# Performance work log

Measured on AMD Instinct MI355X. Metric: run time of the kernel, lower is better.

Reference implementation:

```python
import jax, jax.numpy as jnp
import numpy as np

BINS = 10          # config.bins
SCOPE = 2          # config.dropout_scope_lowest (continue_train=True)
BASE_RATE = 0.0    # self.dropout_rate = zeros(1) when continue_train
THRESH = (BINS - SCOPE) / BINS   # edges[bins - dropout_scope]
UPPER = 1.0 + 1e-6               # edges[bins] (last edge += 1e-6)


def _forward(pred, target, rand_mat, hard_rand, pos_prop):
    B, C = pred.shape
    Bf = jnp.asarray(B, pred.dtype)
    # BCEWithLogits, reduction='none': logaddexp(0,x) - x*t
    bce = jnp.logaddexp(0.0, pred) - pred * target                     # [B,C]
    # g is detached in the torch code
    g = jax.lax.stop_gradient(jnp.abs(jax.nn.sigmoid(pred) - target))  # [B,C]
    # per-class loss -> normalized -> per-class dropout rate
    loss_c = bce.sum(0)                                                # [C]
    ln = jnp.log10(1.0 + loss_c)
    norm = 5.0 - 10.0 * (ln - ln.min()) / (ln.max() - ln.min())
    drate = jnp.maximum(jax.nn.sigmoid(norm), BASE_RATE)               # [C]
    # pos/neg balance bookkeeping (all per-class)
    pos_sum = target.sum(0)                                            # [C]
    neg_sum = Bf - pos_sum
    bal_pos = pos_prop * Bf
    bal_neg = Bf - bal_pos
    pos_gt = pos_sum > bal_pos                                         # majority is positives
    neg_gt = neg_sum > bal_neg                                         # majority is negatives
    balance_num = jnp.where(pos_gt, bal_pos, jnp.where(neg_gt, bal_neg, 0.0))
    dropout_num = jnp.floor(
        jnp.where(pos_gt, pos_sum - bal_pos,
                  jnp.where(neg_gt, neg_sum - bal_neg, 0.0))).astype(jnp.int32)
    # hard/easy class split: uniform(1,C) > dropout_rate
    hard = hard_rand[0] > drate                                        # [C] bool
    maj_lab = pos_gt.astype(pred.dtype)
    min_lab = neg_gt.astype(pred.dtype)
    is_maj = target == maj_lab[None, :]                                # [B,C]
    is_min = target == min_lab[None, :]
    maj_cnt = is_maj.sum(0).astype(pred.dtype)                         # [C]
    min_cnt = is_min.sum(0).astype(pred.dtype)
    # hard branch: reweight majority samples to balance_num/|majority|
    w_hard = jnp.where(is_maj, (balance_num / jnp.maximum(maj_cnt, 1.0))[None, :], 1.0)
    # easy branch: zero the dropout_num easiest (smallest g) majority samples,
    # rescale minority by (B - balance_num)/|minority|
    g_m = jnp.where(is_maj, g, jnp.inf)
    ranks = jnp.argsort(jnp.argsort(g_m, axis=0), axis=0)              # rank among majority by g asc
    drop_easy = is_maj & (ranks < dropout_num[None, :])
    w_easy = jnp.where(is_min & (min_cnt > 0)[None, :],
                       ((Bf - balance_num) / jnp.maximum(min_cnt, 1.0))[None, :], 1.0)
    w_easy = jnp.where(drop_easy, 0.0, w_easy)
    weights = jnp.where(hard[None, :], w_hard, w_easy)                 # [B,C]
    # random dropping of high-|g| (hard-gradient band) samples
    idxs = ((g >= THRESH) & (g < UPPER)).astype(pred.dtype)
    drop_idxs = (rand_mat > drate[None, :]).astype(pred.dtype)
    weights = weights * (1.0 - drop_idxs * idxs)
    return (bce * weights).mean()


def setup_inputs() -> dict:
    key = jax.random.key(0)
    k1, k2, k3, k4, k5 = jax.random.split(key, 5)
    B, C = 131072, 40
    pred = jax.random.normal(k1, (B, C), jnp.float32) * 2.0
    target = jax.random.bernoulli(k2, 0.5, (B, C)).astype(jnp.float32)
    rand_mat = jax.random.uniform(k3, (B, C), jnp.float32)
    hard_rand = jax.random.uniform(k4, (1, C), jnp.float32)
    pos_prop = jax.random.uniform(k5, (C,), jnp.float32, minval=0.3, maxval=0.7)
    return {"pred": pred, "target": target, "rand_mat": rand_mat,
            "hard_rand": hard_rand, "pos_prop": pos_prop}


def reference(pred, target, rand_mat, hard_rand, pos_prop):
    return _forward(pred, target, rand_mat, hard_rand, pos_prop)
```

## Files before the change

### kernel.cpp

```cpp
#include <hip/hip_runtime.h>
#include <hip/hip_bf16.h>
#include <math.h>
#include <stddef.h>

#define BN 131072
#define CN 40
#define NTOT (BN * CN)
#define MASKW (BN / 64)
#define NBLK 1024
#define NCHUNK 8
#define CROWS (BN / NCHUNK)

struct Ws {
    double acc;
    unsigned done;
    unsigned pad0;
    unsigned ghist0[CN][4096];
    unsigned ghist1[CN][1024];
    unsigned ghist2[CN][256];
    double lossc[CN];
    int    posc[CN];
    float drate[CN];
    float majl[CN];
    float minl[CN];
    float w_hard[CN];
    float w_easy[CN];
    int   hardf[CN];
    int   kdrop[CN];
    int   minpos[CN];
    union {
        unsigned long long mask[CN][MASKW];
        struct { float lpart[CN][NBLK]; int ppart[CN][NBLK]; } parts;
    } u;
    unsigned long long eqmask[CN][MASKW];
    unsigned keys[CN][BN];
};

__device__ __forceinline__ float bce_f(float x, float t) {
    float e = __expf(-fabsf(x));
    return fmaxf(x, 0.0f) + __logf(1.0f + e) - x * t;
}
__device__ __forceinline__ float g_f(float x, float t) {
    float e   = __expf(-fabsf(x));
    float inv = __builtin_amdgcn_rcpf(1.0f + e);
    float s   = (x >= 0.0f) ? inv : e * inv;
    return fabsf(s - t);
}
__device__ __forceinline__ void bce_g(float x, float t, float& bce, float& g) {
    float e   = __expf(-fabsf(x));
    bce       = fmaxf(x, 0.0f) + __logf(1.0f + e) - x * t;
    float inv = __builtin_amdgcn_rcpf(1.0f + e);
    float s   = (x >= 0.0f) ? inv : e * inv;
    g         = fabsf(s - t);
}
__device__ __forceinline__ unsigned masked_key(unsigned key, unsigned majb) {
    return ((key & 1u) == majb) ? (key >> 1) : 0xFFFFFFFFu;
}
__device__ __forceinline__ bool col_active(const Ws* ws, int c) {
    return (ws->kdrop[c] > 0) && (ws->hardf[c] == 0);
}

template<int PER, int NBINS>
__device__ __forceinline__ void scan_pick(const unsigned* __restrict__ gh,
                                          unsigned krem,
                                          unsigned* wsum ,
                                          unsigned* out2 ) {
    int tid = threadIdx.x, lane = tid & 63, w = tid >> 6;
    unsigned v[PER];
    unsigned s = 0;
    #pragma unroll
    for (int i = 0; i < PER; ++i) {
        int idx = tid * PER + i;
        v[i] = (idx < NBINS) ? gh[idx] : 0u;
        s += v[i];
    }
    unsigned isc = s;
    #pragma unroll
    for (int d = 1; d < 64; d <<= 1) {
        unsigned o = __shfl_up(isc, (unsigned)d, 64);
        if (lane >= d) isc += o;
    }
    if (lane == 63) wsum[w] = isc;
    __syncthreads();
    unsigned wpre = 0;
    #pragma unroll
    for (int j = 0; j < 16; ++j) wpre += (j < w) ? wsum[j] : 0u;
    unsigned inc = wpre + isc, prev = inc - s;
    if (prev < krem && inc >= krem) {
        unsigned cum = prev;
        #pragma unroll
        for (int i = 0; i < PER; ++i) {
            if (cum < krem && cum + v[i] >= krem) {
                out2[0] = (unsigned)(tid * PER + i);
                out2[1] = krem - cum;
            }
            cum += v[i];
        }
    }
    __syncthreads();
}

__global__ __launch_bounds__(640) void k_fuse(const float* __restrict__ pred,
                                              const float* __restrict__ tgt,
                                              Ws* __restrict__ ws) {
    __shared__ unsigned shk[128 * 41];
    __shared__ float sl[CN];
    __shared__ int   sp[CN];
    int tid = threadIdx.x;
    if (tid < CN) { sl[tid] = 0.0f; sp[tid] = 0; }
    __syncthreads();

    int  tile  = (blockIdx.x & 7) * 128 + (blockIdx.x >> 3);
    long tile0 = (long)tile * 5120;
    int  c0    = (tid * 4) % 40;
    float accl[4] = {0, 0, 0, 0};
    int   cntp[4] = {0, 0, 0, 0};

    #pragma unroll
    for (int j = 0; j < 2; ++j) {
        int e = j * 2560 + tid * 4;
        const float4 p = *(const float4*)(pred + tile0 + e);
        const float4 t = *(const float4*)(tgt + tile0 + e);
        int r = e / 40;
        #pragma unroll
        for (int u = 0; u < 4; ++u) {
            float pu = (&p.x)[u], tu = (&t.x)[u];
            float bce, g;
            bce_g(pu, tu, bce, g);
            accl[u] += bce;
            int tb = (tu != 0.0f) ? 1 : 0;
            cntp[u] += tb;
            shk[r * 41 + c0 + u] = (__float_as_uint(g) << 1) | (unsigned)tb;
        }
    }
    #pragma unroll
    for (int u = 0; u < 4; ++u) {
        atomicAdd(&sl[c0 + u], accl[u]);
        atomicAdd(&sp[c0 + u], cntp[u]);
    }
    __syncthreads();

    int w = tid / 128, r = tid % 128;
    int row0 = tile * 128;
    #pragma unroll
    for (int cc = 0; cc < 8; ++cc) {
        int c = w * 8 + cc;
        ws->keys[c][row0 + r] = shk[r * 41 + c];
    }
    if (tid < CN) {
        ws->u.parts.lpart[tid][blockIdx.x] = sl[tid];
        ws->u.parts.ppart[tid][blockIdx.x] = sp[tid];
    }
}

__global__ __launch_bounds__(1024) void k_sel0(const float* __restrict__ hard_rand,
                                               const float* __restrict__ pos_prop,
                                               Ws* __restrict__ ws) {
    const int bid = blockIdx.x;
    const int c = bid >> 3, chunk = bid & 7;
    const int tid = threadIdx.x, lane = tid & 63, wv = tid >> 6;

    __shared__ unsigned h[4096];
    __shared__ double s_lns[CN];
    __shared__ int s_pos;
    __shared__ int s_active, s_kdrop;
    __shared__ unsigned s_majb;

    for (int j = wv; j < CN; j += 16) {
        double s = 0.0;
        for (int q = lane; q < NBLK; q += 64)
            s += (double)ws->u.parts.lpart[j][q];
        #pragma unroll
        for (int d = 32; d >= 1; d >>= 1) s += __shfl_down(s, d, 64);
        if (lane == 0) s_lns[j] = log10(1.0 + s);
    }
    if (wv == 15) {
        int p = 0;
        for (int q = lane; q < NBLK; q += 64) p += ws->u.parts.ppart[c][q];
        #pragma unroll
        for (int d = 32; d >= 1; d >>= 1) p += __shfl_down(p, d, 64);
        if (lane == 0) s_pos = p;
    }
    __syncthreads();
    if (tid == 0) {
        double mn = s_lns[0], mx = s_lns[0];
        for (int i = 1; i < CN; ++i) { mn = fmin(mn, s_lns[i]); mx = fmax(mx, s_lns[i]); }
        double norm = 5.0 - 10.0 * (s_lns[c] - mn) / (mx - mn);
        float drate = (float)(1.0 / (1.0 + exp(-norm)));
        float Bf = (float)BN;
        float pos_sum = (float)s_pos;
        float neg_sum = Bf - pos_sum;
        float bal_pos = pos_prop[c] * Bf;
        float bal_neg = Bf - bal_pos;
        bool pos_gt = pos_sum > bal_pos;
        bool neg_gt = neg_sum > bal_neg;
        float balance = pos_gt ? bal_pos : (neg_gt ? bal_neg : 0.0f);
        float dnum_f  = pos_gt ? (pos_sum - bal_pos)
                               : (neg_gt ? (neg_sum - bal_neg) : 0.0f);
        int   kdrop   = (int)floorf(dnum_f);
        float majl = pos_gt ? 1.0f : 0.0f;
        float minl = neg_gt ? 1.0f : 0.0f;
        float maj_cnt = (majl == 1.0f) ? pos_sum : neg_sum;
        float min_cnt = (minl == 1.0f) ? pos_sum : neg_sum;
        int hardf = (hard_rand[c] > drate) ? 1 : 0;
        if (chunk == 0) {
            ws->drate[c]  = drate;
            ws->majl[c]   = majl;
            ws->minl[c]   = minl;
            ws->w_hard[c] = balance / fmaxf(maj_cnt, 1.0f);
            ws->w_easy[c] = (Bf - balance) / fmaxf(min_cnt, 1.0f);
            ws->hardf[c]  = hardf;
            ws->kdrop[c]  = kdrop;
            ws->minpos[c] = (min_cnt > 0.0f) ? 1 : 0;
        }
        s_active = (kdrop > 0 && hardf == 0) ? 1 : 0;
        s_kdrop  = kdrop;
        s_majb   = (majl != 0.0f) ? 1u : 0u;
    }
    __syncthreads();
    if (!s_active) return;
    const unsigned majb = s_majb;
    const uint4* kc4 = (const uint4*)(ws->keys[c] + chunk * CROWS);

    for (int i = tid; i < 4096; i += 1024) h[i] = 0;
    __syncthreads();
    for (int b4 = tid; b4 < CROWS / 4; b4 += 1024) {
        uint4 kk = kc4[b4];
        unsigned ks[4] = {kk.x, kk.y, kk.z, kk.w};
        #pragma unroll
        for (int q = 0; q < 4; ++q)
            if ((ks[q] & 1u) == majb) atomicAdd(&h[(ks[q] >> 1) >> 18], 1u);
    }
    __syncthreads();
    for (int i = tid; i < 4096; i += 1024)
        if (h[i]) atomicAdd(&ws->ghist0[c][i], h[i]);
}

__global__ __launch_bounds__(1024) void k_hist1(Ws* __restrict__ ws) {
    int c = blockIdx.x >> 3, chunk = blockIdx.x & 7;
    if (!col_active(ws, c)) return;
    __shared__ unsigned wsum[16];
    __shared__ unsigned out2[2];
    scan_pick<4, 4096>(ws->ghist0[c], (unsigned)ws->kdrop[c], wsum, out2);
    unsigned p0 = out2[0];
    unsigned majb = (ws->majl[c] != 0.0f) ? 1u : 0u;
    const uint4* __restrict__ kc4 = (const uint4*)(ws->keys[c] + chunk * CROWS);
    __shared__ unsigned h[1024];
    int tid = threadIdx.x;
    h[tid] = 0;
    __syncthreads();
    for (int b4 = tid; b4 < CROWS / 4; b4 += 1024) {
        uint4 kk = kc4[b4];
        unsigned ks[4] = {kk.x, kk.y, kk.z, kk.w};
        #pragma unroll
        for (int q = 0; q < 4; ++q)
            if ((ks[q] & 1u) == majb) {
                unsigned mk = ks[q] >> 1;
                if ((mk >> 18) == p0) atomicAdd(&h[(mk >> 8) & 0x3FFu], 1u);
            }
    }
    __syncthreads();
    if (h[tid]) atomicAdd(&ws->ghist1[c][tid], h[tid]);
}

__global__ __launch_bounds__(1024) void k_hist2(Ws* __restrict__ ws) {
    int c = blockIdx.x >> 3, chunk = blockIdx.x & 7;
    if (!col_active(ws, c)) return;
    __shared__ unsigned wsum[16];
    __shared__ unsigned out2[2];
    scan_pick<4, 4096>(ws->ghist0[c], (unsigned)ws->kdrop[c], wsum, out2);
    unsigned p0 = out2[0], krem1 = out2[1];
    scan_pick<1, 1024>(ws->ghist1[c], krem1, wsum, out2);
    unsigned pp = (p0 << 10) | out2[0];
    unsigned majb = (ws->majl[c] != 0.0f) ? 1u : 0u;
    const uint4* __restrict__ kc4 = (const uint4*)(ws->keys[c] + chunk * CROWS);
    __shared__ unsigned h[256];
    int tid = threadIdx.x;
    if (tid < 256) h[tid] = 0;
    __syncthreads();
    for (int b4 = tid; b4 < CROWS / 4; b4 += 1024) {
        uint4 kk = kc4[b4];
        unsigned ks[4] = {kk.x, kk.y, kk.z, kk.w};
        #pragma unroll
        for (int q = 0; q < 4; ++q)
            if ((ks[q] & 1u) == majb) {
                unsigned mk = ks[q] >> 1;
                if ((mk >> 8) == pp) atomicAdd(&h[mk & 0xFFu], 1u);
            }
    }
    __syncthreads();
    if (tid < 256 && h[tid]) atomicAdd(&ws->ghist2[c][tid], h[tid]);
}

__global__ __launch_bounds__(1024) void k_mask(Ws* __restrict__ ws) {
    int c = blockIdx.x >> 3, chunk = blockIdx.x & 7;
    int tid = threadIdx.x;
    unsigned long long* mrow = ws->u.mask[c];
    if (!col_active(ws, c)) {
        if (tid < MASKW / NCHUNK) mrow[chunk * (MASKW / NCHUNK) + tid] = 0ull;
        return;
    }
    __shared__ unsigned wsum[16];
    __shared__ unsigned out2[2];
    scan_pick<4, 4096>(ws->ghist0[c], (unsigned)ws->kdrop[c], wsum, out2);
    unsigned p0 = out2[0], krem1 = out2[1];
    scan_pick<1, 1024>(ws->ghist1[c], krem1, wsum, out2);
    unsigned p1 = out2[0], krem2 = out2[1];
    scan_pick<1, 256>(ws->ghist2[c], krem2, wsum, out2);
    unsigned T = (p0 << 18) | (p1 << 8) | out2[0];

    unsigned majb = (ws->majl[c] != 0.0f) ? 1u : 0u;
    const unsigned* __restrict__ kc = ws->keys[c];
    unsigned long long* erow = ws->eqmask[c];
    int lane = tid & 63, w = tid >> 6;
    int base = chunk * CROWS;
    for (int it = 0; it < CROWS / 1024; ++it) {
        int b = base + it * 1024 + tid;
        unsigned m = masked_key(kc[b], majb);
        unsigned long long blt = __ballot(m < T);
        unsigned long long beq = __ballot(m == T);
        if (lane == 0) {
            int word = (base >> 6) + it * 16 + w;
            mrow[word] = blt;
            erow[word] = beq;
        }
    }
}

__global__ __launch_bounds__(1024) void k_tie(Ws* __restrict__ ws) {
    int c = blockIdx.x;
    if (!col_active(ws, c)) return;
    __shared__ unsigned wsum[16];
    __shared__ unsigned out2[2];
    scan_pick<4, 4096>(ws->ghist0[c], (unsigned)ws->kdrop[c], wsum, out2);
    unsigned krem1 = out2[1];
    scan_pick<1, 1024>(ws->ghist1[c], krem1, wsum, out2);
    unsigned krem2 = out2[1];
    scan_pick<1, 256>(ws->ghist2[c], krem2, wsum, out2);
    unsigned need = out2[1];

    int tid = threadIdx.x, lane = tid & 63, w = tid >> 6;
    const unsigned long long* erow = ws->eqmask[c];
    unsigned long long* mrow = ws->u.mask[c];
    unsigned long long e0 = erow[2 * tid], e1 = erow[2 * tid + 1];
    unsigned pc0 = (unsigned)__popcll(e0), pc1 = (unsigned)__popcll(e1);
    unsigned cnt = pc0 + pc1;
    unsigned isc = cnt;
    #pragma unroll
    for (int d = 1; d < 64; d <<= 1) {
        unsigned o = __shfl_up(isc, (unsigned)d, 64);
        if (lane >= d) isc += o;
    }
    if (lane == 63) wsum[w] = isc;
    __syncthreads();
    unsigned wpre = 0;
    #pragma unroll
    for (int j = 0; j < 16; ++j) wpre += (j < w) ? wsum[j] : 0u;
    unsigned prev = wpre + isc - cnt;
    #pragma unroll
    for (int half = 0; half < 2; ++half) {
        unsigned long long e = half ? e1 : e0;
        unsigned pc = half ? pc1 : pc0;
        unsigned p  = half ? prev + pc0 : prev;
        if (pc > 0 && p < need) {
            unsigned keep = need - p;
            if (keep > pc) keep = pc;
            unsigned long long sel;
            if (keep == pc) sel = e;
            else {
                sel = 0ull;
                unsigned long long m = e;
                for (unsigned i = 0; i < keep; ++i) {
                    unsigned long long lsb = m & (~m + 1ull);
                    sel |= lsb;
                    m ^= lsb;
                }
            }
            mrow[2 * tid + half] |= sel;
        }
    }
}

__global__ __launch_bounds__(640) void k_final3(const float* __restrict__ pred,
                                                const float* __restrict__ tgt,
                                                const float* __restrict__ rnd,
                                                Ws* __restrict__ ws,
                                                float* __restrict__ out) {
    int tid = threadIdx.x;
    long tile0 = (long)blockIdx.x * 5120;
    int  c0    = (tid * 4) % 40;
    float drate[4], majl[4], minl[4], wh[4], we[4];
    int hf[4], mp[4];
    #pragma unroll
    for (int u = 0; u < 4; ++u) {
        int c = c0 + u;
        drate[u] = ws->drate[c]; majl[u] = ws->majl[c]; minl[u] = ws->minl[c];
        wh[u] = ws->w_hard[c];   we[u] = ws->w_easy[c];
        hf[u] = ws->hardf[c];    mp[u] = ws->minpos[c];
    }
    double acc = 0.0;
    #pragma unroll
    for (int j = 0; j < 2; ++j) {
        long i = tile0 + j * 2560 + tid * 4;
        const float4 p  = *(const float4*)(pred + i);
        const float4 t  = *(const float4*)(tgt + i);
        const float4 rr = *(const float4*)(rnd + i);
        int b = (int)(i / 40);
        int wsh = b >> 6, bit = b & 63;
        #pragma unroll
        for (int u = 0; u < 4; ++u) {
            float pu = (&p.x)[u], tu = (&t.x)[u], ru = (&rr.x)[u];
            float bce, g;
            bce_g(pu, tu, bce, g);
            float w;
            if (hf[u]) {
                w = (tu == majl[u]) ? wh[u] : 1.0f;
            } else {
                bool dropped = (ws->u.mask[c0 + u][wsh] >> bit) & 1ull;
                w = dropped ? 0.0f : ((tu == minl[u] && mp[u]) ? we[u] : 1.0f);
            }
            if (g >= 0.8f && g < 1.000001f && ru > drate[u]) w = 0.0f;
            acc += (double)(bce * w);
        }
    }
    __shared__ double sd[640];
    sd[tid] = acc;
    __syncthreads();
    for (int s = 320; s >= 5; s >>= 1) {
        if (tid < s) sd[tid] += sd[tid + s];
        __syncthreads();
    }
    if (tid == 0) {
        double v = sd[0] + sd[1] + sd[2] + sd[3] + sd[4];
        atomicAdd(&ws->acc, v);
        __threadfence();
        unsigned t = atomicAdd(&ws->done, 1u);
        if (t == (unsigned)(NBLK - 1)) {
            double total = atomicAdd(&ws->acc, 0.0);
            out[0] = (float)(total / (double)NTOT);
        }
    }
}

__global__ void k_colreduce(const float* __restrict__ pred,
                            const float* __restrict__ tgt,
                            Ws* __restrict__ ws) {
    __shared__ float sl[CN];
    __shared__ int   sp[CN];
    int tid = threadIdx.x;
    if (tid < CN) { sl[tid] = 0.0f; sp[tid] = 0; }
    __syncthreads();
    int stride = gridDim.x * blockDim.x;
    for (int i = blockIdx.x * blockDim.x + tid; i < NTOT; i += stride) {
        int c = i % CN;
        float p = pred[i], t = tgt[i];
        atomicAdd(&sl[c], bce_f(p, t));
        if (t != 0.0f) atomicAdd(&sp[c], 1);
    }
    __syncthreads();
    if (tid < CN) {
        atomicAdd(&ws->lossc[tid], (double)sl[tid]);
        atomicAdd(&ws->posc[tid], sp[tid]);
    }
}

__global__ __launch_bounds__(1024) void k_params(const float* __restrict__ hard_rand,
                                                 const float* __restrict__ pos_prop,
                                                 Ws* __restrict__ ws) {
    int tid = threadIdx.x;
    __shared__ double lns[CN];
    __shared__ double smn, smx;
    if (tid < CN) lns[tid] = log10(1.0 + ws->lossc[tid]);
    __syncthreads();
    if (tid == 0) {
        double a = lns[0], b = lns[0];
        for (int i = 1; i < CN; i++) { a = fmin(a, lns[i]); b = fmax(b, lns[i]); }
        smn = a; smx = b;
    }
    __syncthreads();
    if (tid < CN) {
        int c = tid;
        double norm = 5.0 - 10.0 * (lns[c] - smn) / (smx - smn);
        float drate = (float)(1.0 / (1.0 + exp(-norm)));
        float Bf = (float)BN;
        float pos_sum = (float)ws->posc[c];
        float neg_sum = Bf - pos_sum;
        float bal_pos = pos_prop[c] * Bf;
        float bal_neg = Bf - bal_pos;
        bool pos_gt = pos_sum > bal_pos;
        bool neg_gt = neg_sum > bal_neg;
        float balance = pos_gt ? bal_pos : (neg_gt ? bal_neg : 0.0f);
        float dnum_f  = pos_gt ? (pos_sum - bal_pos)
                               : (neg_gt ? (neg_sum - bal_neg) : 0.0f);
        int   kdrop   = (int)floorf(dnum_f);
        float majl = pos_gt ? 1.0f : 0.0f;
        float minl = neg_gt ? 1.0f : 0.0f;
        float maj_cnt = (majl == 1.0f) ? pos_sum : neg_sum;
        float min_cnt = (minl == 1.0f) ? pos_sum : neg_sum;
        ws->drate[c]  = drate;
        ws->majl[c]   = majl;
        ws->minl[c]   = minl;
        ws->w_hard[c] = balance / fmaxf(maj_cnt, 1.0f);
        ws->w_easy[c] = (Bf - balance) / fmaxf(min_cnt, 1.0f);
        ws->hardf[c]  = (hard_rand[c] > drate) ? 1 : 0;
        ws->kdrop[c]  = kdrop;
        ws->minpos[c] = (min_cnt > 0.0f) ? 1 : 0;
    }
}

__global__ __launch_bounds__(1024) void k_select(const float* __restrict__ pred,
                                                 const float* __restrict__ tgt,
                                                 Ws* __restrict__ ws) {
    int c   = blockIdx.x;
    int tid = threadIdx.x;
    int k   = ws->kdrop[c];
    bool easy = (ws->hardf[c] == 0);
    unsigned long long* mrow = ws->u.mask[c];
    if (k <= 0 || !easy) {
        for (int i = tid; i < MASKW; i += 1024) mrow[i] = 0ull;
        return;
    }
    float majl = ws->majl[c];
    __shared__ unsigned h[256];
    __shared__ unsigned cum[256];
    __shared__ unsigned sh_sel, sh_krem;
    unsigned prefix = 0;
    unsigned krem   = (unsigned)k;
    for (int level = 0; level < 4; ++level) {
        int shift = 24 - 8 * level;
        for (int i = tid; i < 256; i += 1024) h[i] = 0;
        __syncthreads();
        for (int b = tid; b < BN; b += 1024) {
            float t = tgt[b * CN + c];
            if (t == majl) {
                unsigned bits = __float_as_uint(g_f(pred[b * CN + c], t));
                bool ok = (level == 0) || ((bits >> (shift + 8)) == prefix);
                if (ok) atomicAdd(&h[(bits >> shift) & 0xFFu], 1u);
            }
        }
        __syncthreads();
        if (tid < 256) cum[tid] = h[tid];
        __syncthreads();
        for (int off = 1; off < 256; off <<= 1) {
            unsigned v = 0;
            if (tid < 256 && tid >= off) v = cum[tid - off];
            __syncthreads();
            if (tid < 256 && tid >= off) cum[tid] += v;
            __syncthreads();
        }
        if (tid < 256) {
            unsigned prev = (tid == 0) ? 0u : cum[tid - 1];
            if (cum[tid] >= krem && prev < krem) {
                sh_sel  = (unsigned)tid;
                sh_krem = krem - prev;
            }
        }
        __syncthreads();
        prefix = (prefix << 8) | sh_sel;
        krem   = sh_krem;
        __syncthreads();
    }
    unsigned T    = prefix;
    unsigned need = krem;
    __shared__ unsigned wcnt[16];
    unsigned base = 0;
    int lane = tid & 63, wid = tid >> 6;
    for (int chunk = 0; chunk < BN / 1024; ++chunk) {
        int b = chunk * 1024 + tid;
        float t = tgt[b * CN + c];
        bool ismaj = (t == majl);
        unsigned bits = 0xFFFFFFFFu;
        if (ismaj) bits = __float_as_uint(g_f(pred[b * CN + c], t));
        bool lt = ismaj && (bits < T);
        bool eq = ismaj && (bits == T);
        unsigned long long bal = __ballot(eq);
        if (lane == 0) wcnt[wid] = (unsigned)__popcll(bal);
        __syncthreads();
        unsigned woff = 0, tot = 0;
        for (int w = 0; w < 16; ++w) {
            unsigned v = wcnt[w];
            if (w < wid) woff += v;
            tot += v;
        }
        unsigned long long lanemask = (lane == 0) ? 0ull : ((~0ull) >> (64 - lane));
        unsigned myrank = base + woff + (unsigned)__popcll(bal & lanemask);
        bool dropped = lt || (eq && myrank < need);
        unsigned long long bd = __ballot(dropped);
        if (lane == 0) mrow[chunk * 16 + wid] = bd;
        base += tot;
        __syncthreads();
    }
}

__global__ void k_final(const float* __restrict__ pred,
                        const float* __restrict__ tgt,
                        const float* __restrict__ rnd,
                        Ws* __restrict__ ws) {
    __shared__ double sdata[256];
    double acc = 0.0;
    int stride = gridDim.x * blockDim.x;
    for (int i = blockIdx.x * blockDim.x + threadIdx.x; i < NTOT; i += stride) {
        int b = i / CN;
        int c = i - b * CN;
        float p = pred[i], t = tgt[i], r = rnd[i];
        float bce = bce_f(p, t);
        float g   = g_f(p, t);
        float w;
        if (ws->hardf[c]) {
            w = (t == ws->majl[c]) ? ws->w_hard[c] : 1.0f;
        } else {
            bool dropped = (ws->u.mask[c][b >> 6] >> (b & 63)) & 1ull;
            if (dropped) w = 0.0f;
            else w = ((t == ws->minl[c]) && ws->minpos[c]) ? ws->w_easy[c] : 1.0f;
        }
        if ((g >= 0.8f) && (g < 1.000001f) && (r > ws->drate[c])) w = 0.0f;
        acc += (double)(bce * w);
    }
    sdata[threadIdx.x] = acc;
    __syncthreads();
    for (int s = blockDim.x / 2; s > 0; s >>= 1) {
        if (threadIdx.x < s) sdata[threadIdx.x] += sdata[threadIdx.x + s];
        __syncthreads();
    }
    if (threadIdx.x == 0) atomicAdd(&ws->acc, sdata[0]);
}

__global__ void k_write(Ws* __restrict__ ws, float* __restrict__ out) {
    out[0] = (float)(ws->acc / (double)NTOT);
}

extern "C" void kernel_launch(void* const* d_in, const int* in_sizes, int n_in,
                              void* d_out, int out_size, void* d_ws, size_t ws_size,
                              hipStream_t stream) {
    const float* pred      = (const float*)d_in[0];
    const float* tgt       = (const float*)d_in[1];
    const float* rnd       = (const float*)d_in[2];
    const float* hard_rand = (const float*)d_in[3];
    const float* pos_prop  = (const float*)d_in[4];
    Ws* ws = (Ws*)d_ws;

    if (ws_size >= sizeof(Ws)) {
        hipMemsetAsync(d_ws, 0, offsetof(Ws, lossc), stream);
        k_fuse  <<<NBLK, 640, 0, stream>>>(pred, tgt, ws);
        k_sel0  <<<CN * NCHUNK, 1024, 0, stream>>>(hard_rand, pos_prop, ws);
        k_hist1 <<<CN * NCHUNK, 1024, 0, stream>>>(ws);
        k_hist2 <<<CN * NCHUNK, 1024, 0, stream>>>(ws);
        k_mask  <<<CN * NCHUNK, 1024, 0, stream>>>(ws);
        k_tie   <<<CN, 1024, 0, stream>>>(ws);
        k_final3<<<NBLK, 640, 0, stream>>>(pred, tgt, rnd, ws, (float*)d_out);
    } else {
        hipMemsetAsync(d_ws, 0, offsetof(Ws, drate), stream);
        k_colreduce<<<2048, 256, 0, stream>>>(pred, tgt, ws);
        k_params<<<1, 1024, 0, stream>>>(hard_rand, pos_prop, ws);
        k_select<<<CN, 1024, 0, stream>>>(pred, tgt, ws);
        k_final <<<2048, 256, 0, stream>>>(pred, tgt, rnd, ws);
        k_write <<<1, 1, 0, stream>>>(ws, (float*)d_out);
    }
}
```

Baseline: 202.0 us.

## Split per-column param reduction into single-block kernel and stage final params/mask in LDS

The per-column parameter reduction that every one of the 320 sel0 blocks used to recompute redundantly (summing all 40x1024 loss partials) moves into a single-block k_params2 kernel. A separate k_hist0 kernel then does only the histogram work. k_final3 now preloads per-column parameters and its two mask words per column into shared memory instead of reading them from global memory inside the inner loop. The cost is one extra kernel launch and a serial single-block stage in exchange for removing redundant reduction work.

```diff
diff --git a/kernel.cpp b/kernel.cpp
--- a/kernel.cpp
+++ b/kernel.cpp
@@ -153,42 +153,45 @@
     }
 }
 
-__global__ __launch_bounds__(1024) void k_sel0(const float* __restrict__ hard_rand,
-                                               const float* __restrict__ pos_prop,
-                                               Ws* __restrict__ ws) {
-    const int bid = blockIdx.x;
-    const int c = bid >> 3, chunk = bid & 7;
-    const int tid = threadIdx.x, lane = tid & 63, wv = tid >> 6;
-
-    __shared__ unsigned h[4096];
-    __shared__ double s_lns[CN];
-    __shared__ int s_pos;
-    __shared__ int s_active, s_kdrop;
-    __shared__ unsigned s_majb;
-
-    for (int j = wv; j < CN; j += 16) {
-        double s = 0.0;
-        for (int q = lane; q < NBLK; q += 64)
-            s += (double)ws->u.parts.lpart[j][q];
-        #pragma unroll
-        for (int d = 32; d >= 1; d >>= 1) s += __shfl_down(s, d, 64);
-        if (lane == 0) s_lns[j] = log10(1.0 + s);
-    }
-    if (wv == 15) {
-        int p = 0;
-        for (int q = lane; q < NBLK; q += 64) p += ws->u.parts.ppart[c][q];
-        #pragma unroll
-        for (int d = 32; d >= 1; d >>= 1) p += __shfl_down(p, d, 64);
-        if (lane == 0) s_pos = p;
+__global__ __launch_bounds__(1024) void k_params2(const float* __restrict__ hard_rand,
+                                                  const float* __restrict__ pos_prop,
+                                                  Ws* __restrict__ ws) {
+    int tid = threadIdx.x;
+    __shared__ double sred[CN][17];
+    __shared__ int    spre[CN][17];
+    __shared__ double lossv[CN];
+    __shared__ int    posv[CN];
+    __shared__ double lns[CN];
+    __shared__ double smn, smx;
+    if (tid < CN * 16) {
+        int c = tid >> 4, j = tid & 15;
+        double s = 0.0; int p = 0;
+        for (int i = j; i < NBLK; i += 16) {
+            s += (double)ws->u.parts.lpart[c][i];
+            p += ws->u.parts.ppart[c][i];
+        }
+        sred[c][j] = s; spre[c][j] = p;
+    }
+    __syncthreads();
+    if (tid < CN) {
+        double s = 0.0; int p = 0;
+        for (int j = 0; j < 16; ++j) { s += sred[tid][j]; p += spre[tid][j]; }
+        lossv[tid] = s; posv[tid] = p;
+        lns[tid] = log10(1.0 + s);
     }
     __syncthreads();
     if (tid == 0) {
-        double mn = s_lns[0], mx = s_lns[0];
-        for (int i = 1; i < CN; ++i) { mn = fmin(mn, s_lns[i]); mx = fmax(mx, s_lns[i]); }
-        double norm = 5.0 - 10.0 * (s_lns[c] - mn) / (mx - mn);
+        double a = lns[0], b = lns[0];
+        for (int i = 1; i < CN; i++) { a = fmin(a, lns[i]); b = fmax(b, lns[i]); }
+        smn = a; smx = b;
+    }
+    __syncthreads();
+    if (tid < CN) {
+        int c = tid;
+        double norm = 5.0 - 10.0 * (lns[c] - smn) / (smx - smn);
         float drate = (float)(1.0 / (1.0 + exp(-norm)));
         float Bf = (float)BN;
-        float pos_sum = (float)s_pos;
+        float pos_sum = (float)posv[c];
         float neg_sum = Bf - pos_sum;
         float bal_pos = pos_prop[c] * Bf;
         float bal_neg = Bf - bal_pos;
@@ -202,26 +205,24 @@
         float minl = neg_gt ? 1.0f : 0.0f;
         float maj_cnt = (majl == 1.0f) ? pos_sum : neg_sum;
         float min_cnt = (minl == 1.0f) ? pos_sum : neg_sum;
-        int hardf = (hard_rand[c] > drate) ? 1 : 0;
-        if (chunk == 0) {
-            ws->drate[c]  = drate;
-            ws->majl[c]   = majl;
-            ws->minl[c]   = minl;
-            ws->w_hard[c] = balance / fmaxf(maj_cnt, 1.0f);
-            ws->w_easy[c] = (Bf - balance) / fmaxf(min_cnt, 1.0f);
-            ws->hardf[c]  = hardf;
-            ws->kdrop[c]  = kdrop;
-            ws->minpos[c] = (min_cnt > 0.0f) ? 1 : 0;
-        }
-        s_active = (kdrop > 0 && hardf == 0) ? 1 : 0;
-        s_kdrop  = kdrop;
-        s_majb   = (majl != 0.0f) ? 1u : 0u;
-    }
-    __syncthreads();
-    if (!s_active) return;
-    const unsigned majb = s_majb;
-    const uint4* kc4 = (const uint4*)(ws->keys[c] + chunk * CROWS);
-
+        ws->drate[c]  = drate;
+        ws->majl[c]   = majl;
+        ws->minl[c]   = minl;
+        ws->w_hard[c] = balance / fmaxf(maj_cnt, 1.0f);
+        ws->w_easy[c] = (Bf - balance) / fmaxf(min_cnt, 1.0f);
+        ws->hardf[c]  = (hard_rand[c] > drate) ? 1 : 0;
+        ws->kdrop[c]  = kdrop;
+        ws->minpos[c] = (min_cnt > 0.0f) ? 1 : 0;
+    }
+}
+
+__global__ __launch_bounds__(1024) void k_hist0(Ws* __restrict__ ws) {
+    int c = blockIdx.x >> 3, chunk = blockIdx.x & 7;
+    if (!col_active(ws, c)) return;
+    unsigned majb = (ws->majl[c] != 0.0f) ? 1u : 0u;
+    const uint4* __restrict__ kc4 = (const uint4*)(ws->keys[c] + chunk * CROWS);
+    __shared__ unsigned h[4096];
+    int tid = threadIdx.x;
     for (int i = tid; i < 4096; i += 1024) h[i] = 0;
     __syncthreads();
     for (int b4 = tid; b4 < CROWS / 4; b4 += 1024) {
@@ -386,7 +387,23 @@
                                                 const float* __restrict__ rnd,
                                                 Ws* __restrict__ ws,
                                                 float* __restrict__ out) {
-    int tid = threadIdx.x;
+    __shared__ double sd[640];
+    __shared__ unsigned long long smask[CN][2];
+    __shared__ float sdrate[CN], smajl[CN], sminl[CN], swh[CN], swe[CN];
+    __shared__ int shf[CN], smp[CN];
+    int tid = threadIdx.x;
+    if (tid < CN) {
+        sdrate[tid] = ws->drate[tid]; smajl[tid] = ws->majl[tid];
+        sminl[tid]  = ws->minl[tid];  swh[tid]  = ws->w_hard[tid];
+        swe[tid]    = ws->w_easy[tid]; shf[tid] = ws->hardf[tid];
+        smp[tid]    = ws->minpos[tid];
+    }
+    if (tid >= 64 && tid < 64 + 2 * CN) {
+        int q = tid - 64;
+        smask[q >> 1][q & 1] = ws->u.mask[q >> 1][blockIdx.x * 2 + (q & 1)];
+    }
+    __syncthreads();
+
     long tile0 = (long)blockIdx.x * 5120;
     int  c0    = (tid * 4) % 40;
     float drate[4], majl[4], minl[4], wh[4], we[4];
@@ -394,9 +411,9 @@
     #pragma unroll
     for (int u = 0; u < 4; ++u) {
         int c = c0 + u;
-        drate[u] = ws->drate[c]; majl[u] = ws->majl[c]; minl[u] = ws->minl[c];
-        wh[u] = ws->w_hard[c];   we[u] = ws->w_easy[c];
-        hf[u] = ws->hardf[c];    mp[u] = ws->minpos[c];
+        drate[u] = sdrate[c]; majl[u] = smajl[c]; minl[u] = sminl[c];
+        wh[u] = swh[c];       we[u] = swe[c];
+        hf[u] = shf[c];       mp[u] = smp[c];
     }
     double acc = 0.0;
     #pragma unroll
@@ -406,7 +423,7 @@
         const float4 t  = *(const float4*)(tgt + i);
         const float4 rr = *(const float4*)(rnd + i);
         int b = (int)(i / 40);
-        int wsh = b >> 6, bit = b & 63;
+        int bit = b & 63;
         #pragma unroll
         for (int u = 0; u < 4; ++u) {
             float pu = (&p.x)[u], tu = (&t.x)[u], ru = (&rr.x)[u];
@@ -416,14 +433,13 @@
             if (hf[u]) {
                 w = (tu == majl[u]) ? wh[u] : 1.0f;
             } else {
-                bool dropped = (ws->u.mask[c0 + u][wsh] >> bit) & 1ull;
+                bool dropped = (smask[c0 + u][j] >> bit) & 1ull;
                 w = dropped ? 0.0f : ((tu == minl[u] && mp[u]) ? we[u] : 1.0f);
             }
             if (g >= 0.8f && g < 1.000001f && ru > drate[u]) w = 0.0f;
             acc += (double)(bce * w);
         }
     }
-    __shared__ double sd[640];
     sd[tid] = acc;
     __syncthreads();
     for (int s = 320; s >= 5; s >>= 1) {
@@ -641,13 +657,14 @@
 
     if (ws_size >= sizeof(Ws)) {
         hipMemsetAsync(d_ws, 0, offsetof(Ws, lossc), stream);
-        k_fuse  <<<NBLK, 640, 0, stream>>>(pred, tgt, ws);
-        k_sel0  <<<CN * NCHUNK, 1024, 0, stream>>>(hard_rand, pos_prop, ws);
-        k_hist1 <<<CN * NCHUNK, 1024, 0, stream>>>(ws);
-        k_hist2 <<<CN * NCHUNK, 1024, 0, stream>>>(ws);
-        k_mask  <<<CN * NCHUNK, 1024, 0, stream>>>(ws);
-        k_tie   <<<CN, 1024, 0, stream>>>(ws);
-        k_final3<<<NBLK, 640, 0, stream>>>(pred, tgt, rnd, ws, (float*)d_out);
+        k_fuse   <<<NBLK, 640, 0, stream>>>(pred, tgt, ws);
+        k_params2<<<1, 1024, 0, stream>>>(hard_rand, pos_prop, ws);
+        k_hist0  <<<CN * NCHUNK, 1024, 0, stream>>>(ws);
+        k_hist1  <<<CN * NCHUNK, 1024, 0, stream>>>(ws);
+        k_hist2  <<<CN * NCHUNK, 1024, 0, stream>>>(ws);
+        k_mask   <<<CN * NCHUNK, 1024, 0, stream>>>(ws);
+        k_tie    <<<CN, 1024, 0, stream>>>(ws);
+        k_final3 <<<NBLK, 640, 0, stream>>>(pred, tgt, rnd, ws, (float*)d_out);
     } else {
         hipMemsetAsync(d_ws, 0, offsetof(Ws, drate), stream);
         k_colreduce<<<2048, 256, 0, stream>>>(pred, tgt, ws);
```

After: 201.1 us. About the same (-0.4%).

## Replace bitmask selection with per-column threshold key and row tie-break

Applied to the files above, without the earlier changes.

Reworks the per-column top-k drop selection. The radix passes become 11/12/7 bits, with the last pass folding row-high bits into the histogram so ties resolve to an exact row threshold. The per-element mask and eqmask writes and the k_mask and k_tie kernels are replaced by a single k_thresh kernel that finds (mkT, rowT). The final kernel then recomputes the drop decision from g and the row index instead of reading a 40x131072-bit mask. This removes a full mask write/read pass and one launch, adds a separate param-reduction kernel, and changes the final kernel to 2048 blocks of 320 threads with per-column parameters staged in shared memory.

```diff
diff --git a/kernel.cpp b/kernel.cpp
--- a/kernel.cpp
+++ b/kernel.cpp
@@ -8,6 +8,7 @@
 #define NTOT (BN * CN)
 #define MASKW (BN / 64)
 #define NBLK 1024
+#define NFIN 2048
 #define NCHUNK 8
 #define CROWS (BN / NCHUNK)
 
@@ -15,9 +16,12 @@
     double acc;
     unsigned done;
     unsigned pad0;
-    unsigned ghist0[CN][4096];
-    unsigned ghist1[CN][1024];
-    unsigned ghist2[CN][256];
+    unsigned ghist0[CN][2048];
+    union {
+        struct { unsigned h1[CN][4096]; unsigned h2[CN][4096]; } g;
+        struct { float lpart[CN][NBLK]; int ppart[CN][NBLK]; } parts;
+        unsigned long long mask[CN][MASKW];
+    } u;
     double lossc[CN];
     int    posc[CN];
     float drate[CN];
@@ -28,11 +32,9 @@
     int   hardf[CN];
     int   kdrop[CN];
     int   minpos[CN];
-    union {
-        unsigned long long mask[CN][MASKW];
-        struct { float lpart[CN][NBLK]; int ppart[CN][NBLK]; } parts;
-    } u;
-    unsigned long long eqmask[CN][MASKW];
+    unsigned mkT[CN];
+    unsigned rowT[CN];
+    int      en[CN];
     unsigned keys[CN][BN];
 };
 
@@ -52,9 +54,6 @@
     float inv = __builtin_amdgcn_rcpf(1.0f + e);
     float s   = (x >= 0.0f) ? inv : e * inv;
     g         = fabsf(s - t);
-}
-__device__ __forceinline__ unsigned masked_key(unsigned key, unsigned majb) {
-    return ((key & 1u) == majb) ? (key >> 1) : 0xFFFFFFFFu;
 }
 __device__ __forceinline__ bool col_active(const Ws* ws, int c) {
     return (ws->kdrop[c] > 0) && (ws->hardf[c] == 0);
@@ -153,42 +152,43 @@
     }
 }
 
-__global__ __launch_bounds__(1024) void k_sel0(const float* __restrict__ hard_rand,
-                                               const float* __restrict__ pos_prop,
-                                               Ws* __restrict__ ws) {
-    const int bid = blockIdx.x;
-    const int c = bid >> 3, chunk = bid & 7;
-    const int tid = threadIdx.x, lane = tid & 63, wv = tid >> 6;
-
-    __shared__ unsigned h[4096];
-    __shared__ double s_lns[CN];
-    __shared__ int s_pos;
-    __shared__ int s_active, s_kdrop;
+__global__ __launch_bounds__(256) void k_paramsA(Ws* __restrict__ ws) {
+    int c = blockIdx.x, tid = threadIdx.x;
+    __shared__ double sd[256];
+    __shared__ int    si[256];
+    double s = 0.0; int p = 0;
+    for (int i = tid; i < NBLK; i += 256) {
+        s += (double)ws->u.parts.lpart[c][i];
+        p += ws->u.parts.ppart[c][i];
+    }
+    sd[tid] = s; si[tid] = p;
+    __syncthreads();
+    for (int st = 128; st > 0; st >>= 1) {
+        if (tid < st) { sd[tid] += sd[tid + st]; si[tid] += si[tid + st]; }
+        __syncthreads();
+    }
+    if (tid == 0) { ws->lossc[c] = sd[0]; ws->posc[c] = si[0]; }
+}
+
+__global__ __launch_bounds__(1024) void k_h0(const float* __restrict__ hard_rand,
+                                             const float* __restrict__ pos_prop,
+                                             Ws* __restrict__ ws) {
+    const int bid = blockIdx.x, c = bid >> 3, chunk = bid & 7;
+    const int tid = threadIdx.x;
+    ((unsigned*)&ws->u.g)[bid * 1024 + tid] = 0;
+
+    __shared__ double lns[CN];
+    __shared__ int s_active;
     __shared__ unsigned s_majb;
-
-    for (int j = wv; j < CN; j += 16) {
-        double s = 0.0;
-        for (int q = lane; q < NBLK; q += 64)
-            s += (double)ws->u.parts.lpart[j][q];
-        #pragma unroll
-        for (int d = 32; d >= 1; d >>= 1) s += __shfl_down(s, d, 64);
-        if (lane == 0) s_lns[j] = log10(1.0 + s);
-    }
-    if (wv == 15) {
-        int p = 0;
-        for (int q = lane; q < NBLK; q += 64) p += ws->u.parts.ppart[c][q];
-        #pragma unroll
-        for (int d = 32; d >= 1; d >>= 1) p += __shfl_down(p, d, 64);
-        if (lane == 0) s_pos = p;
-    }
+    if (tid < CN) lns[tid] = log10(1.0 + ws->lossc[tid]);
     __syncthreads();
     if (tid == 0) {
-        double mn = s_lns[0], mx = s_lns[0];
-        for (int i = 1; i < CN; ++i) { mn = fmin(mn, s_lns[i]); mx = fmax(mx, s_lns[i]); }
-        double norm = 5.0 - 10.0 * (s_lns[c] - mn) / (mx - mn);
+        double mn = lns[0], mx = lns[0];
+        for (int i = 1; i < CN; ++i) { mn = fmin(mn, lns[i]); mx = fmax(mx, lns[i]); }
+        double norm = 5.0 - 10.0 * (lns[c] - mn) / (mx - mn);
         float drate = (float)(1.0 / (1.0 + exp(-norm)));
         float Bf = (float)BN;
-        float pos_sum = (float)s_pos;
+        float pos_sum = (float)ws->posc[c];
         float neg_sum = Bf - pos_sum;
         float bal_pos = pos_prop[c] * Bf;
         float bal_neg = Bf - bal_pos;
@@ -214,40 +214,39 @@
             ws->minpos[c] = (min_cnt > 0.0f) ? 1 : 0;
         }
         s_active = (kdrop > 0 && hardf == 0) ? 1 : 0;
-        s_kdrop  = kdrop;
         s_majb   = (majl != 0.0f) ? 1u : 0u;
     }
     __syncthreads();
     if (!s_active) return;
     const unsigned majb = s_majb;
-    const uint4* kc4 = (const uint4*)(ws->keys[c] + chunk * CROWS);
-
-    for (int i = tid; i < 4096; i += 1024) h[i] = 0;
+    const uint4* __restrict__ kc4 = (const uint4*)(ws->keys[c] + chunk * CROWS);
+    __shared__ unsigned h[2048];
+    h[tid] = 0; h[tid + 1024] = 0;
     __syncthreads();
     for (int b4 = tid; b4 < CROWS / 4; b4 += 1024) {
         uint4 kk = kc4[b4];
         unsigned ks[4] = {kk.x, kk.y, kk.z, kk.w};
         #pragma unroll
         for (int q = 0; q < 4; ++q)
-            if ((ks[q] & 1u) == majb) atomicAdd(&h[(ks[q] >> 1) >> 18], 1u);
-    }
-    __syncthreads();
-    for (int i = tid; i < 4096; i += 1024)
-        if (h[i]) atomicAdd(&ws->ghist0[c][i], h[i]);
-}
-
-__global__ __launch_bounds__(1024) void k_hist1(Ws* __restrict__ ws) {
+            if ((ks[q] & 1u) == majb) atomicAdd(&h[(ks[q] >> 1) >> 19], 1u);
+    }
+    __syncthreads();
+    if (h[tid])        atomicAdd(&ws->ghist0[c][tid], h[tid]);
+    if (h[tid + 1024]) atomicAdd(&ws->ghist0[c][tid + 1024], h[tid + 1024]);
+}
+
+__global__ __launch_bounds__(1024) void k_h1(Ws* __restrict__ ws) {
     int c = blockIdx.x >> 3, chunk = blockIdx.x & 7;
     if (!col_active(ws, c)) return;
     __shared__ unsigned wsum[16];
     __shared__ unsigned out2[2];
-    scan_pick<4, 4096>(ws->ghist0[c], (unsigned)ws->kdrop[c], wsum, out2);
+    scan_pick<2, 2048>(ws->ghist0[c], (unsigned)ws->kdrop[c], wsum, out2);
     unsigned p0 = out2[0];
     unsigned majb = (ws->majl[c] != 0.0f) ? 1u : 0u;
     const uint4* __restrict__ kc4 = (const uint4*)(ws->keys[c] + chunk * CROWS);
-    __shared__ unsigned h[1024];
+    __shared__ unsigned h[4096];
     int tid = threadIdx.x;
-    h[tid] = 0;
+    for (int i = tid; i < 4096; i += 1024) h[i] = 0;
     __syncthreads();
     for (int b4 = tid; b4 < CROWS / 4; b4 += 1024) {
         uint4 kk = kc4[b4];
@@ -256,28 +255,30 @@
         for (int q = 0; q < 4; ++q)
             if ((ks[q] & 1u) == majb) {
                 unsigned mk = ks[q] >> 1;
-                if ((mk >> 18) == p0) atomicAdd(&h[(mk >> 8) & 0x3FFu], 1u);
+                if ((mk >> 19) == p0) atomicAdd(&h[(mk >> 7) & 0xFFFu], 1u);
             }
     }
     __syncthreads();
-    if (h[tid]) atomicAdd(&ws->ghist1[c][tid], h[tid]);
-}
-
-__global__ __launch_bounds__(1024) void k_hist2(Ws* __restrict__ ws) {
+    for (int i = tid; i < 4096; i += 1024)
+        if (h[i]) atomicAdd(&ws->u.g.h1[c][i], h[i]);
+}
+
+__global__ __launch_bounds__(1024) void k_h2(Ws* __restrict__ ws) {
     int c = blockIdx.x >> 3, chunk = blockIdx.x & 7;
     if (!col_active(ws, c)) return;
     __shared__ unsigned wsum[16];
     __shared__ unsigned out2[2];
-    scan_pick<4, 4096>(ws->ghist0[c], (unsigned)ws->kdrop[c], wsum, out2);
+    scan_pick<2, 2048>(ws->ghist0[c], (unsigned)ws->kdrop[c], wsum, out2);
     unsigned p0 = out2[0], krem1 = out2[1];
-    scan_pick<1, 1024>(ws->ghist1[c], krem1, wsum, out2);
-    unsigned pp = (p0 << 10) | out2[0];
+    scan_pick<4, 4096>(ws->u.g.h1[c], krem1, wsum, out2);
+    unsigned p01 = (p0 << 12) | out2[0];
     unsigned majb = (ws->majl[c] != 0.0f) ? 1u : 0u;
     const uint4* __restrict__ kc4 = (const uint4*)(ws->keys[c] + chunk * CROWS);
-    __shared__ unsigned h[256];
+    __shared__ unsigned h[4096];
     int tid = threadIdx.x;
-    if (tid < 256) h[tid] = 0;
-    __syncthreads();
+    for (int i = tid; i < 4096; i += 1024) h[i] = 0;
+    __syncthreads();
+    int rbase = chunk * CROWS;
     for (int b4 = tid; b4 < CROWS / 4; b4 += 1024) {
         uint4 kk = kc4[b4];
         unsigned ks[4] = {kk.x, kk.y, kk.z, kk.w};
@@ -285,148 +286,132 @@
         for (int q = 0; q < 4; ++q)
             if ((ks[q] & 1u) == majb) {
                 unsigned mk = ks[q] >> 1;
-                if ((mk >> 8) == pp) atomicAdd(&h[mk & 0xFFu], 1u);
+                if ((mk >> 7) == p01) {
+                    unsigned row = (unsigned)(rbase + b4 * 4 + q);
+                    atomicAdd(&h[((mk & 0x7Fu) << 5) | (row >> 12)], 1u);
+                }
             }
     }
     __syncthreads();
-    if (tid < 256 && h[tid]) atomicAdd(&ws->ghist2[c][tid], h[tid]);
-}
-
-__global__ __launch_bounds__(1024) void k_mask(Ws* __restrict__ ws) {
-    int c = blockIdx.x >> 3, chunk = blockIdx.x & 7;
-    int tid = threadIdx.x;
-    unsigned long long* mrow = ws->u.mask[c];
+    for (int i = tid; i < 4096; i += 1024)
+        if (h[i]) atomicAdd(&ws->u.g.h2[c][i], h[i]);
+}
+
+__global__ __launch_bounds__(1024) void k_thresh(Ws* __restrict__ ws) {
+    int c = blockIdx.x, tid = threadIdx.x;
     if (!col_active(ws, c)) {
-        if (tid < MASKW / NCHUNK) mrow[chunk * (MASKW / NCHUNK) + tid] = 0ull;
+        if (tid == 0) { ws->en[c] = 0; ws->mkT[c] = 0; ws->rowT[c] = 0; }
         return;
     }
     __shared__ unsigned wsum[16];
     __shared__ unsigned out2[2];
-    scan_pick<4, 4096>(ws->ghist0[c], (unsigned)ws->kdrop[c], wsum, out2);
+    scan_pick<2, 2048>(ws->ghist0[c], (unsigned)ws->kdrop[c], wsum, out2);
     unsigned p0 = out2[0], krem1 = out2[1];
-    scan_pick<1, 1024>(ws->ghist1[c], krem1, wsum, out2);
+    scan_pick<4, 4096>(ws->u.g.h1[c], krem1, wsum, out2);
     unsigned p1 = out2[0], krem2 = out2[1];
-    scan_pick<1, 256>(ws->ghist2[c], krem2, wsum, out2);
-    unsigned T = (p0 << 18) | (p1 << 8) | out2[0];
-
+    scan_pick<4, 4096>(ws->u.g.h2[c], krem2, wsum, out2);
+    unsigned p2 = out2[0], krem3 = out2[1];
+
+    unsigned mkT = ((((p0 << 12) | p1)) << 7) | (p2 >> 5);
+    unsigned rowHi = p2 & 0x1Fu;
+    unsigned base = rowHi << 12;
     unsigned majb = (ws->majl[c] != 0.0f) ? 1u : 0u;
     const unsigned* __restrict__ kc = ws->keys[c];
-    unsigned long long* erow = ws->eqmask[c];
+
+    __shared__ unsigned wcnt[16];
+    __shared__ unsigned s_row;
     int lane = tid & 63, w = tid >> 6;
-    int base = chunk * CROWS;
-    for (int it = 0; it < CROWS / 1024; ++it) {
-        int b = base + it * 1024 + tid;
-        unsigned m = masked_key(kc[b], majb);
-        unsigned long long blt = __ballot(m < T);
-        unsigned long long beq = __ballot(m == T);
-        if (lane == 0) {
-            int word = (base >> 6) + it * 16 + w;
-            mrow[word] = blt;
-            erow[word] = beq;
-        }
-    }
-}
-
-__global__ __launch_bounds__(1024) void k_tie(Ws* __restrict__ ws) {
-    int c = blockIdx.x;
-    if (!col_active(ws, c)) return;
-    __shared__ unsigned wsum[16];
-    __shared__ unsigned out2[2];
-    scan_pick<4, 4096>(ws->ghist0[c], (unsigned)ws->kdrop[c], wsum, out2);
-    unsigned krem1 = out2[1];
-    scan_pick<1, 1024>(ws->ghist1[c], krem1, wsum, out2);
-    unsigned krem2 = out2[1];
-    scan_pick<1, 256>(ws->ghist2[c], krem2, wsum, out2);
-    unsigned need = out2[1];
-
-    int tid = threadIdx.x, lane = tid & 63, w = tid >> 6;
-    const unsigned long long* erow = ws->eqmask[c];
-    unsigned long long* mrow = ws->u.mask[c];
-    unsigned long long e0 = erow[2 * tid], e1 = erow[2 * tid + 1];
-    unsigned pc0 = (unsigned)__popcll(e0), pc1 = (unsigned)__popcll(e1);
-    unsigned cnt = pc0 + pc1;
-    unsigned isc = cnt;
-    #pragma unroll
-    for (int d = 1; d < 64; d <<= 1) {
-        unsigned o = __shfl_up(isc, (unsigned)d, 64);
-        if (lane >= d) isc += o;
-    }
-    if (lane == 63) wsum[w] = isc;
-    __syncthreads();
-    unsigned wpre = 0;
-    #pragma unroll
-    for (int j = 0; j < 16; ++j) wpre += (j < w) ? wsum[j] : 0u;
-    unsigned prev = wpre + isc - cnt;
-    #pragma unroll
-    for (int half = 0; half < 2; ++half) {
-        unsigned long long e = half ? e1 : e0;
-        unsigned pc = half ? pc1 : pc0;
-        unsigned p  = half ? prev + pc0 : prev;
-        if (pc > 0 && p < need) {
-            unsigned keep = need - p;
-            if (keep > pc) keep = pc;
-            unsigned long long sel;
-            if (keep == pc) sel = e;
-            else {
-                sel = 0ull;
-                unsigned long long m = e;
-                for (unsigned i = 0; i < keep; ++i) {
-                    unsigned long long lsb = m & (~m + 1ull);
-                    sel |= lsb;
-                    m ^= lsb;
-                }
-            }
-            mrow[2 * tid + half] |= sel;
-        }
-    }
-}
-
-__global__ __launch_bounds__(640) void k_final3(const float* __restrict__ pred,
+    unsigned cum = 0;
+    unsigned long long lanemask = (lane == 0) ? 0ull : ((~0ull) >> (64 - lane));
+    for (int it = 0; it < 4; ++it) {
+        unsigned row = base + it * 1024 + tid;
+        unsigned key = kc[row];
+        bool eq = ((key & 1u) == majb) && ((key >> 1) == mkT);
+        unsigned long long bal = __ballot(eq);
+        if (lane == 0) wcnt[w] = (unsigned)__popcll(bal);
+        __syncthreads();
+        unsigned woff = 0, tot = 0;
+        for (int j = 0; j < 16; ++j) {
+            unsigned v = wcnt[j];
+            if (j < w) woff += v;
+            tot += v;
+        }
+        unsigned myrank = cum + woff + (unsigned)__popcll(bal & lanemask);
+        if (eq && myrank == krem3 - 1) s_row = row;
+        cum += tot;
+        __syncthreads();
+    }
+    if (tid == 0) { ws->en[c] = 1; ws->mkT[c] = mkT; ws->rowT[c] = s_row; }
+}
+
+__global__ __launch_bounds__(320) void k_final4(const float* __restrict__ pred,
                                                 const float* __restrict__ tgt,
                                                 const float* __restrict__ rnd,
                                                 Ws* __restrict__ ws,
                                                 float* __restrict__ out) {
+    __shared__ double sd[320];
+    __shared__ float sdr[CN], smj[CN], smn[CN], swh[CN], swe[CN];
+    __shared__ int shf[CN], smp[CN], sen[CN];
+    __shared__ unsigned skT[CN], srT[CN];
     int tid = threadIdx.x;
-    long tile0 = (long)blockIdx.x * 5120;
-    int  c0    = (tid * 4) % 40;
+    if (tid < CN) {
+        sdr[tid] = ws->drate[tid]; smj[tid] = ws->majl[tid];
+        smn[tid] = ws->minl[tid];  swh[tid] = ws->w_hard[tid];
+        swe[tid] = ws->w_easy[tid]; shf[tid] = ws->hardf[tid];
+        smp[tid] = ws->minpos[tid]; sen[tid] = ws->en[tid];
+        skT[tid] = ws->mkT[tid];   srT[tid] = ws->rowT[tid];
+    }
+    __syncthreads();
+
+    long i0 = (long)blockIdx.x * 2560 + tid * 4;
+    const float4 pA = *(const float4*)(pred + i0);
+    const float4 tA = *(const float4*)(tgt + i0);
+    const float4 rA = *(const float4*)(rnd + i0);
+    const float4 pB = *(const float4*)(pred + i0 + 1280);
+    const float4 tB = *(const float4*)(tgt + i0 + 1280);
+    const float4 rB = *(const float4*)(rnd + i0 + 1280);
+
+    int c0 = (tid * 4) % 40;
+    unsigned b0 = (unsigned)(i0 / 40);
     float drate[4], majl[4], minl[4], wh[4], we[4];
-    int hf[4], mp[4];
+    int hf[4], mp[4], en[4];
+    unsigned mkT[4], rowT[4];
     #pragma unroll
     for (int u = 0; u < 4; ++u) {
         int c = c0 + u;
-        drate[u] = ws->drate[c]; majl[u] = ws->majl[c]; minl[u] = ws->minl[c];
-        wh[u] = ws->w_hard[c];   we[u] = ws->w_easy[c];
-        hf[u] = ws->hardf[c];    mp[u] = ws->minpos[c];
+        drate[u] = sdr[c]; majl[u] = smj[c]; minl[u] = smn[c];
+        wh[u] = swh[c]; we[u] = swe[c];
+        hf[u] = shf[c]; mp[u] = smp[c]; en[u] = sen[c];
+        mkT[u] = skT[c]; rowT[u] = srT[c];
     }
     double acc = 0.0;
     #pragma unroll
     for (int j = 0; j < 2; ++j) {
-        long i = tile0 + j * 2560 + tid * 4;
-        const float4 p  = *(const float4*)(pred + i);
-        const float4 t  = *(const float4*)(tgt + i);
-        const float4 rr = *(const float4*)(rnd + i);
-        int b = (int)(i / 40);
-        int wsh = b >> 6, bit = b & 63;
+        const float4& p = j ? pB : pA;
+        const float4& t = j ? tB : tA;
+        const float4& r = j ? rB : rA;
+        unsigned b = b0 + (j ? 32u : 0u);
         #pragma unroll
         for (int u = 0; u < 4; ++u) {
-            float pu = (&p.x)[u], tu = (&t.x)[u], ru = (&rr.x)[u];
+            float pu = (&p.x)[u], tu = (&t.x)[u], ru = (&r.x)[u];
             float bce, g;
             bce_g(pu, tu, bce, g);
             float w;
             if (hf[u]) {
                 w = (tu == majl[u]) ? wh[u] : 1.0f;
             } else {
-                bool dropped = (ws->u.mask[c0 + u][wsh] >> bit) & 1ull;
+                unsigned mk = __float_as_uint(g);
+                bool dropped = (tu == majl[u]) && en[u] &&
+                               (mk < mkT[u] || (mk == mkT[u] && b <= rowT[u]));
                 w = dropped ? 0.0f : ((tu == minl[u] && mp[u]) ? we[u] : 1.0f);
             }
             if (g >= 0.8f && g < 1.000001f && ru > drate[u]) w = 0.0f;
             acc += (double)(bce * w);
         }
     }
-    __shared__ double sd[640];
     sd[tid] = acc;
     __syncthreads();
-    for (int s = 320; s >= 5; s >>= 1) {
+    for (int s = 160; s >= 5; s >>= 1) {
         if (tid < s) sd[tid] += sd[tid + s];
         __syncthreads();
     }
@@ -435,7 +420,7 @@
         atomicAdd(&ws->acc, v);
         __threadfence();
         unsigned t = atomicAdd(&ws->done, 1u);
-        if (t == (unsigned)(NBLK - 1)) {
+        if (t == (unsigned)(NFIN - 1)) {
             double total = atomicAdd(&ws->acc, 0.0);
             out[0] = (float)(total / (double)NTOT);
         }
@@ -640,16 +625,17 @@
     Ws* ws = (Ws*)d_ws;
 
     if (ws_size >= sizeof(Ws)) {
-        hipMemsetAsync(d_ws, 0, offsetof(Ws, lossc), stream);
-        k_fuse  <<<NBLK, 640, 0, stream>>>(pred, tgt, ws);
-        k_sel0  <<<CN * NCHUNK, 1024, 0, stream>>>(hard_rand, pos_prop, ws);
-        k_hist1 <<<CN * NCHUNK, 1024, 0, stream>>>(ws);
-        k_hist2 <<<CN * NCHUNK, 1024, 0, stream>>>(ws);
-        k_mask  <<<CN * NCHUNK, 1024, 0, stream>>>(ws);
-        k_tie   <<<CN, 1024, 0, stream>>>(ws);
-        k_final3<<<NBLK, 640, 0, stream>>>(pred, tgt, rnd, ws, (float*)d_out);
+        hipMemsetAsync(d_ws, 0, offsetof(Ws, u), stream);
+        k_fuse   <<<NBLK, 640, 0, stream>>>(pred, tgt, ws);
+        k_paramsA<<<CN, 256, 0, stream>>>(ws);
+        k_h0     <<<CN * NCHUNK, 1024, 0, stream>>>(hard_rand, pos_prop, ws);
+        k_h1     <<<CN * NCHUNK, 1024, 0, stream>>>(ws);
+        k_h2     <<<CN * NCHUNK, 1024, 0, stream>>>(ws);
+        k_thresh <<<CN, 1024, 0, stream>>>(ws);
+        k_final4 <<<NFIN, 320, 0, stream>>>(pred, tgt, rnd, ws, (float*)d_out);
     } else {
-        hipMemsetAsync(d_ws, 0, offsetof(Ws, drate), stream);
+        hipMemsetAsync(d_ws, 0, offsetof(Ws, u), stream);
+        hipMemsetAsync(&((Ws*)d_ws)->lossc, 0, sizeof(double) * CN + sizeof(int) * CN, stream);
         k_colreduce<<<2048, 256, 0, stream>>>(pred, tgt, ws);
         k_params<<<1, 1024, 0, stream>>>(hard_rand, pos_prop, ws);
         k_select<<<CN, 1024, 0, stream>>>(pred, tgt, ws);
```

New measurement: 207.1 us. 2.5% more time.
